# Kernel optimization log

Hardware: AMD Instinct MI355X
Metric: run time of the kernel (lower is better)

The kernel has to match this reference:

```python
import jax, jax.numpy as jnp
import numpy as np

N_NODES = 50000
N_EDGES = 800000
D_IN = 128
D_OUT = 128
ALPHA = 0.5


def setup_inputs() -> dict:
    key = jax.random.key(0)
    k1, k2, k3, k4, k5, k6 = jax.random.split(key, 6)
    x = jax.random.normal(k1, (N_NODES, D_IN), dtype=jnp.float32)
    edge_index = jax.random.randint(k2, (2, N_EDGES), 0, N_NODES, dtype=jnp.int32)
    s = 1.0 / np.sqrt(D_IN)  # torch.nn.Linear default init bound
    W_src = jax.random.uniform(k3, (D_IN, D_OUT), jnp.float32, -s, s)
    b_src = jax.random.uniform(k4, (D_OUT,), jnp.float32, -s, s)
    W_dst = jax.random.uniform(k5, (D_IN, D_OUT), jnp.float32, -s, s)
    b_dst = jax.random.uniform(k6, (D_OUT,), jnp.float32, -s, s)
    return {"x": x, "edge_index": edge_index, "W_src": W_src, "b_src": b_src,
            "W_dst": W_dst, "b_dst": b_dst}


def reference(x, edge_index, W_src, b_src, W_dst, b_dst):
    row, col = edge_index[0], edge_index[1]
    ones = jnp.ones((row.shape[0],), dtype=x.dtype)
    # out-degree = row sums of A; in-degree = column sums of A
    out_deg = jax.ops.segment_sum(ones, row, num_segments=N_NODES)
    in_deg = jax.ops.segment_sum(ones, col, num_segments=N_NODES)
    d_out = jnp.where(out_deg > 0, out_deg ** -0.5, 0.0)
    d_in = jnp.where(in_deg > 0, in_deg ** -0.5, 0.0)
    # D_out^{-1/2} A D_in^{-1/2}: per-edge weight. For A^T the normalized
    # weight at (col,row) is d_in[col]*d_out[row] == same weight, transposed scatter.
    w = d_out[row] * d_in[col]  # [E]
    msg_fwd = w[:, None] * x[col]  # [E, D_IN]
    agg_fwd = jax.ops.segment_sum(msg_fwd, row, num_segments=N_NODES)  # adj_norm @ x
    msg_bwd = w[:, None] * x[row]
    agg_bwd = jax.ops.segment_sum(msg_bwd, col, num_segments=N_NODES)  # adj_t_norm @ x
    out = ALPHA * (agg_fwd @ W_src + b_src) + (1.0 - ALPHA) * (agg_bwd @ W_dst + b_dst)
    return out
```

## Files before the change

### kernel.cpp

```cpp
#include <hip/hip_runtime.h>
#include <hip/hip_bf16.h>


constexpr int N_NODES = 50000;
constexpr int N_EDGES = 800000;
constexpr int D = 128;
constexpr int CAP = 48;
constexpr int NPBK = 512;
constexpr int NBUK = (N_NODES + NPBK - 1) / NPBK;
constexpr int ECH = 2048;
constexpr int NCH = (N_EDGES + ECH - 1) / ECH;
constexpr int CAPB = 12288;

typedef __bf16 bf16x8 __attribute__((ext_vector_type(8)));
typedef float  f32x4  __attribute__((ext_vector_type(4)));

__global__ __launch_bounds__(256) void k_part(const int* __restrict__ row,
                                              const int* __restrict__ col,
                                              int* __restrict__ tail,
                                              unsigned* __restrict__ part,
                                              const float* __restrict__ Wsrc,
                                              const float* __restrict__ Wdst,
                                              __hip_bfloat16* __restrict__ Wpk) {
    const int bid = blockIdx.x;
    if (bid >= NCH * 2) {
        int tid = (bid - NCH * 2) * 256 + threadIdx.x;
        int f = tid >> 6;
        int lane = tid & 63;
        int dir = f >> 5;
        int ct = (f >> 2) & 7;
        int ks = f & 3;
        const float* W = dir ? Wdst : Wsrc;
        int k0 = ks * 32 + (lane >> 4) * 8;
        int n = ct * 16 + (lane & 15);
        __hip_bfloat16 v[8];
        #pragma unroll
        for (int j = 0; j < 8; ++j) v[j] = __float2bfloat16(W[(k0 + j) * D + n]);
        *(bf16x8*)&Wpk[(size_t)tid * 8] = *(const bf16x8*)v;
        return;
    }
    __shared__ int cnt[NBUK], base[NBUK], pos[NBUK];
    const int dir = bid & 1;
    const int chunk = bid >> 1;
    const int* dst = dir ? col : row;
    const int* src = dir ? row : col;
    for (int i = threadIdx.x; i < NBUK; i += 256) { cnt[i] = 0; pos[i] = 0; }
    __syncthreads();
    const int e0 = chunk * ECH;
    const int e1 = min(e0 + ECH, N_EDGES);
    for (int e = e0 + threadIdx.x; e < e1; e += 256)
        atomicAdd(&cnt[dst[e] >> 9], 1);
    __syncthreads();
    for (int i = threadIdx.x; i < NBUK; i += 256)
        base[i] = (cnt[i] > 0) ? atomicAdd(&tail[dir * NBUK + i], cnt[i]) : 0;
    __syncthreads();
    for (int e = e0 + threadIdx.x; e < e1; e += 256) {
        int d = dst[e], s = src[e];
        int b = d >> 9;
        int p = base[b] + atomicAdd(&pos[b], 1);
        if (p < CAPB)
            part[((size_t)dir * NBUK + b) * CAPB + p] =
                ((unsigned)(d & (NPBK - 1)) << 16) | (unsigned)s;
    }
}

__global__ __launch_bounds__(256) void k_bin(const int* __restrict__ tail,
                                             const unsigned* __restrict__ part,
                                             unsigned short* __restrict__ binF,
                                             unsigned short* __restrict__ binB,
                                             int* __restrict__ cntF,
                                             int* __restrict__ cntB,
                                             float* __restrict__ sc_row,
                                             float* __restrict__ sc_col) {
    __shared__ alignas(16) unsigned short bins[NPBK * CAP];
    __shared__ int cnt[NPBK];
    const int dir = blockIdx.x & 1;
    const int b = blockIdx.x >> 1;
    for (int i = threadIdx.x; i < NPBK; i += 256) cnt[i] = 0;
    __syncthreads();
    const int n = min(tail[dir * NBUK + b], CAPB);
    const unsigned* p = &part[((size_t)dir * NBUK + b) * CAPB];
    for (int i = threadIdx.x; i < n; i += 256) {
        unsigned ent = p[i];
        int dl = ent >> 16;
        int q = atomicAdd(&cnt[dl], 1);
        if (q < CAP) bins[dl * CAP + q] = (unsigned short)(ent & 0xFFFFu);
    }
    __syncthreads();
    unsigned short* gbin = dir ? binB : binF;
    int* gcnt = dir ? cntB : cntF;
    float* sc = dir ? sc_col : sc_row;
    const int node0 = b * NPBK;
    const int nv = min(NPBK, N_NODES - node0);
    const int nq = nv * (CAP * 2 / 16);
    const uint4* bw = (const uint4*)bins;
    uint4* gw = (uint4*)&gbin[(size_t)node0 * CAP];
    for (int i = threadIdx.x; i < nq; i += 256) gw[i] = bw[i];
    for (int i = threadIdx.x; i < nv; i += 256) {
        int c = cnt[i];
        gcnt[node0 + i] = c;
        sc[node0 + i] = (c > 0) ? rsqrtf((float)c) : 0.f;
    }
}

__global__ __launch_bounds__(256) void k_gemm_mfma(const float* __restrict__ x,
                                                   const bf16x8* __restrict__ Wpk,
                                                   const float* __restrict__ sc_col,
                                                   const float* __restrict__ sc_row,
                                                   __hip_bfloat16* __restrict__ hF,
                                                   __hip_bfloat16* __restrict__ hB) {
    __shared__ bf16x8 Bs[64 * 64];
    for (int i = threadIdx.x; i < 64 * 64; i += 256) Bs[i] = Wpk[i];

    const int wave = threadIdx.x >> 6;
    const int lane = threadIdx.x & 63;
    const int quad = lane >> 4;
    const int m0 = blockIdx.x * 64 + wave * 16;

    const int arow = min(m0 + (lane & 15), N_NODES - 1);
    bf16x8 a[4];
    #pragma unroll
    for (int ks = 0; ks < 4; ++ks) {
        const float* px = &x[(size_t)arow * D + ks * 32 + quad * 8];
        float4 v0 = *(const float4*)px;
        float4 v1 = *(const float4*)(px + 4);
        union { bf16x8 v; __hip_bfloat16 e[8]; } u;
        u.e[0] = __float2bfloat16(v0.x); u.e[1] = __float2bfloat16(v0.y);
        u.e[2] = __float2bfloat16(v0.z); u.e[3] = __float2bfloat16(v0.w);
        u.e[4] = __float2bfloat16(v1.x); u.e[5] = __float2bfloat16(v1.y);
        u.e[6] = __float2bfloat16(v1.z); u.e[7] = __float2bfloat16(v1.w);
        a[ks] = u.v;
    }

    const int crow = m0 + quad * 4;
    float fF[4], fB[4];
    #pragma unroll
    for (int r = 0; r < 4; ++r) {
        int nd = min(crow + r, N_NODES - 1);
        fF[r] = 0.5f * sc_col[nd];
        fB[r] = 0.5f * sc_row[nd];
    }

    __syncthreads();

    #pragma unroll
    for (int ct = 0; ct < 8; ++ct) {
        f32x4 cF = {0.f, 0.f, 0.f, 0.f};
        f32x4 cB = {0.f, 0.f, 0.f, 0.f};
        #pragma unroll
        for (int ks = 0; ks < 4; ++ks) {
            bf16x8 bF = Bs[(ct * 4 + ks) * 64 + lane];
            bf16x8 bB = Bs[(32 + ct * 4 + ks) * 64 + lane];
            cF = __builtin_amdgcn_mfma_f32_16x16x32_bf16(a[ks], bF, cF, 0, 0, 0);
            cB = __builtin_amdgcn_mfma_f32_16x16x32_bf16(a[ks], bB, cB, 0, 0, 0);
        }
        const int colb = ct * 16 + (lane & 15);
        #pragma unroll
        for (int r = 0; r < 4; ++r) {
            int nd = crow + r;
            if (nd < N_NODES) {
                hF[(size_t)nd * D + colb] = __float2bfloat16(fF[r] * cF[r]);
                hB[(size_t)nd * D + colb] = __float2bfloat16(fB[r] * cB[r]);
            }
        }
    }
}

__device__ __forceinline__ float4 bf4_to_f4(uint2 u) {
    union { unsigned i; float f; } a, b, c, d;
    a.i = u.x << 16;
    b.i = u.x & 0xFFFF0000u;
    c.i = u.y << 16;
    d.i = u.y & 0xFFFF0000u;
    return make_float4(a.f, b.f, c.f, d.f);
}

__global__ __launch_bounds__(256) void k_gather(const unsigned short* __restrict__ binF,
                                                const int* __restrict__ cntF,
                                                const unsigned short* __restrict__ binB,
                                                const int* __restrict__ cntB,
                                                const float* __restrict__ sc_row,
                                                const float* __restrict__ sc_col,
                                                const uint2* __restrict__ hF,
                                                const uint2* __restrict__ hB,
                                                const float* __restrict__ b_src,
                                                const float* __restrict__ b_dst,
                                                float* __restrict__ out) {
    const int node = blockIdx.x * 4 + (threadIdx.x >> 6);
    const int lane = threadIdx.x & 63;
    const int half = lane >> 5;
    const int l32 = lane & 31;
    const int nF = min(cntF[node], CAP);
    const int nB = min(cntB[node], CAP);

    int entF = (lane < nF) ? (int)binF[(size_t)node * CAP + lane] : 0;
    int entB = (lane < nB) ? (int)binB[(size_t)node * CAP + lane] : 0;

    const int sTailF = __shfl(entF, (nF > 0) ? nF - 1 : 0);
    const int sTailB = __shfl(entB, (nB > 0) ? nB - 1 : 0);

    float4 accF = make_float4(0.f, 0.f, 0.f, 0.f);
    {
        const int npair = nF >> 1;
        int i = 0;
        for (; i + 3 < npair; i += 4) {
            int s0 = __shfl(entF, 2 * i + half);
            int s1 = __shfl(entF, 2 * (i + 1) + half);
            int s2 = __shfl(entF, 2 * (i + 2) + half);
            int s3 = __shfl(entF, 2 * (i + 3) + half);
            uint2 v0 = hF[(size_t)s0 * 32 + l32];
            uint2 v1 = hF[(size_t)s1 * 32 + l32];
            uint2 v2 = hF[(size_t)s2 * 32 + l32];
            uint2 v3 = hF[(size_t)s3 * 32 + l32];
            float4 f0 = bf4_to_f4(v0), f1 = bf4_to_f4(v1);
            float4 f2 = bf4_to_f4(v2), f3 = bf4_to_f4(v3);
            accF.x += (f0.x + f1.x) + (f2.x + f3.x);
            accF.y += (f0.y + f1.y) + (f2.y + f3.y);
            accF.z += (f0.z + f1.z) + (f2.z + f3.z);
            accF.w += (f0.w + f1.w) + (f2.w + f3.w);
        }
        for (; i < npair; ++i) {
            int s = __shfl(entF, 2 * i + half);
            float4 f = bf4_to_f4(hF[(size_t)s * 32 + l32]);
            accF.x += f.x; accF.y += f.y; accF.z += f.z; accF.w += f.w;
        }
        if ((nF & 1) && half == 0) {
            float4 f = bf4_to_f4(hF[(size_t)sTailF * 32 + l32]);
            accF.x += f.x; accF.y += f.y; accF.z += f.z; accF.w += f.w;
        }
    }
    float4 accB = make_float4(0.f, 0.f, 0.f, 0.f);
    {
        const int npair = nB >> 1;
        int i = 0;
        for (; i + 3 < npair; i += 4) {
            int s0 = __shfl(entB, 2 * i + half);
            int s1 = __shfl(entB, 2 * (i + 1) + half);
            int s2 = __shfl(entB, 2 * (i + 2) + half);
            int s3 = __shfl(entB, 2 * (i + 3) + half);
            uint2 v0 = hB[(size_t)s0 * 32 + l32];
            uint2 v1 = hB[(size_t)s1 * 32 + l32];
            uint2 v2 = hB[(size_t)s2 * 32 + l32];
            uint2 v3 = hB[(size_t)s3 * 32 + l32];
            float4 f0 = bf4_to_f4(v0), f1 = bf4_to_f4(v1);
            float4 f2 = bf4_to_f4(v2), f3 = bf4_to_f4(v3);
            accB.x += (f0.x + f1.x) + (f2.x + f3.x);
            accB.y += (f0.y + f1.y) + (f2.y + f3.y);
            accB.z += (f0.z + f1.z) + (f2.z + f3.z);
            accB.w += (f0.w + f1.w) + (f2.w + f3.w);
        }
        for (; i < npair; ++i) {
            int s = __shfl(entB, 2 * i + half);
            float4 f = bf4_to_f4(hB[(size_t)s * 32 + l32]);
            accB.x += f.x; accB.y += f.y; accB.z += f.z; accB.w += f.w;
        }
        if ((nB & 1) && half == 0) {
            float4 f = bf4_to_f4(hB[(size_t)sTailB * 32 + l32]);
            accB.x += f.x; accB.y += f.y; accB.z += f.z; accB.w += f.w;
        }
    }

    accF.x += __shfl_xor(accF.x, 32);
    accF.y += __shfl_xor(accF.y, 32);
    accF.z += __shfl_xor(accF.z, 32);
    accF.w += __shfl_xor(accF.w, 32);
    accB.x += __shfl_xor(accB.x, 32);
    accB.y += __shfl_xor(accB.y, 32);
    accB.z += __shfl_xor(accB.z, 32);
    accB.w += __shfl_xor(accB.w, 32);

    if (half == 0) {
        float4 bs = *(const float4*)&b_src[l32 * 4];
        float4 bd = *(const float4*)&b_dst[l32 * 4];
        float sF = sc_row[node];
        float sB = sc_col[node];
        float4 o;
        o.x = 0.5f * (bs.x + bd.x) + sF * accF.x + sB * accB.x;
        o.y = 0.5f * (bs.y + bd.y) + sF * accF.y + sB * accB.y;
        o.z = 0.5f * (bs.z + bd.z) + sF * accF.z + sB * accB.z;
        o.w = 0.5f * (bs.w + bd.w) + sF * accF.w + sB * accB.w;
        *(float4*)&out[(size_t)node * D + l32 * 4] = o;
    }
}

extern "C" void kernel_launch(void* const* d_in, const int* in_sizes, int n_in,
                              void* d_out, int out_size, void* d_ws, size_t ws_size,
                              hipStream_t stream) {
    const float* x     = (const float*)d_in[0];
    const int*   edges = (const int*)d_in[1];
    const float* W_src = (const float*)d_in[2];
    const float* b_src = (const float*)d_in[3];
    const float* W_dst = (const float*)d_in[4];
    const float* b_dst = (const float*)d_in[5];
    float* out = (float*)d_out;

    const int* row = edges;
    const int* col = edges + N_EDGES;

    __hip_bfloat16* hFu    = (__hip_bfloat16*)d_ws;
    __hip_bfloat16* hBu    = hFu + (size_t)N_NODES * D;
    __hip_bfloat16* Wpk    = hBu + (size_t)N_NODES * D;
    float*          sc_row = (float*)(Wpk + 64 * 512);
    float*          sc_col = sc_row + N_NODES;
    int*            cntF   = (int*)(sc_col + N_NODES);
    int*            cntB   = cntF + N_NODES;
    int*            tail   = cntB + N_NODES;
    unsigned*       part   = (unsigned*)(tail + 256);
    unsigned short* binF   = (unsigned short*)(part + (size_t)2 * NBUK * CAPB);
    unsigned short* binB   = binF + (size_t)N_NODES * CAP;

    (void)hipMemsetAsync(tail, 0, 256 * sizeof(int), stream);

    const int gP = NCH * 2 + 16;
    const int gB = NBUK * 2;
    const int gM = (N_NODES + 63) / 64;
    const int gG = N_NODES / 4;

    k_part<<<gP, 256, 0, stream>>>(row, col, tail, part, W_src, W_dst, Wpk);
    k_bin<<<gB, 256, 0, stream>>>(tail, part, binF, binB, cntF, cntB, sc_row, sc_col);
    k_gemm_mfma<<<gM, 256, 0, stream>>>(x, (const bf16x8*)Wpk, sc_col, sc_row, hFu, hBu);
    k_gather<<<gG, 256, 0, stream>>>(binF, cntF, binB, cntB, sc_row, sc_col,
                                     (const uint2*)hFu, (const uint2*)hBu,
                                     b_src, b_dst, out);
}
```

Before: 197.1 us.

## Aggregate before GEMM: gather bf16 x once, then fused dual-weight MFMA GEMM

Reorders the computation to aggregate first and multiply by the weights afterwards. Previously the code projected x through both weight matrices into two bf16 feature tables and then gathered from each. Now x is converted to bf16 once inside the partition kernel, the gather reads that single table for both directions with per-edge source scaling, and a final MFMA kernel multiplies the concatenated aggregates by [W_src; W_dst] and adds the bias. This halves the working set of the random gather. The cost is per-edge weight shuffles, an extra write and read of the aggregates, and reuse of the partition buffer's memory for aggF.

```diff
diff --git a/kernel.cpp b/kernel.cpp
--- a/kernel.cpp
+++ b/kernel.cpp
@@ -11,6 +11,7 @@
 constexpr int ECH = 2048;
 constexpr int NCH = (N_EDGES + ECH - 1) / ECH;
 constexpr int CAPB = 12288;
+constexpr int CVTB = 128;
 
 typedef __bf16 bf16x8 __attribute__((ext_vector_type(8)));
 typedef float  f32x4  __attribute__((ext_vector_type(4)));
@@ -21,8 +22,27 @@
                                               unsigned* __restrict__ part,
                                               const float* __restrict__ Wsrc,
                                               const float* __restrict__ Wdst,
-                                              __hip_bfloat16* __restrict__ Wpk) {
+                                              __hip_bfloat16* __restrict__ Wpk,
+                                              const float* __restrict__ x,
+                                              __hip_bfloat16* __restrict__ xb) {
     const int bid = blockIdx.x;
+    if (bid >= NCH * 2 + 16) {
+        const float4* x4 = (const float4*)x;
+        bf16x8* xb8 = (bf16x8*)xb;
+        const int stride = CVTB * 256;
+        for (int i = (bid - (NCH * 2 + 16)) * 256 + threadIdx.x;
+             i < N_NODES * D / 8; i += stride) {
+            float4 v0 = x4[2 * i];
+            float4 v1 = x4[2 * i + 1];
+            union { bf16x8 v; __hip_bfloat16 e[8]; } u;
+            u.e[0] = __float2bfloat16(v0.x); u.e[1] = __float2bfloat16(v0.y);
+            u.e[2] = __float2bfloat16(v0.z); u.e[3] = __float2bfloat16(v0.w);
+            u.e[4] = __float2bfloat16(v1.x); u.e[5] = __float2bfloat16(v1.y);
+            u.e[6] = __float2bfloat16(v1.z); u.e[7] = __float2bfloat16(v1.w);
+            xb8[i] = u.v;
+        }
+        return;
+    }
     if (bid >= NCH * 2) {
         int tid = (bid - NCH * 2) * 256 + threadIdx.x;
         int f = tid >> 6;
@@ -103,69 +123,6 @@
     }
 }
 
-__global__ __launch_bounds__(256) void k_gemm_mfma(const float* __restrict__ x,
-                                                   const bf16x8* __restrict__ Wpk,
-                                                   const float* __restrict__ sc_col,
-                                                   const float* __restrict__ sc_row,
-                                                   __hip_bfloat16* __restrict__ hF,
-                                                   __hip_bfloat16* __restrict__ hB) {
-    __shared__ bf16x8 Bs[64 * 64];
-    for (int i = threadIdx.x; i < 64 * 64; i += 256) Bs[i] = Wpk[i];
-
-    const int wave = threadIdx.x >> 6;
-    const int lane = threadIdx.x & 63;
-    const int quad = lane >> 4;
-    const int m0 = blockIdx.x * 64 + wave * 16;
-
-    const int arow = min(m0 + (lane & 15), N_NODES - 1);
-    bf16x8 a[4];
-    #pragma unroll
-    for (int ks = 0; ks < 4; ++ks) {
-        const float* px = &x[(size_t)arow * D + ks * 32 + quad * 8];
-        float4 v0 = *(const float4*)px;
-        float4 v1 = *(const float4*)(px + 4);
-        union { bf16x8 v; __hip_bfloat16 e[8]; } u;
-        u.e[0] = __float2bfloat16(v0.x); u.e[1] = __float2bfloat16(v0.y);
-        u.e[2] = __float2bfloat16(v0.z); u.e[3] = __float2bfloat16(v0.w);
-        u.e[4] = __float2bfloat16(v1.x); u.e[5] = __float2bfloat16(v1.y);
-        u.e[6] = __float2bfloat16(v1.z); u.e[7] = __float2bfloat16(v1.w);
-        a[ks] = u.v;
-    }
-
-    const int crow = m0 + quad * 4;
-    float fF[4], fB[4];
-    #pragma unroll
-    for (int r = 0; r < 4; ++r) {
-        int nd = min(crow + r, N_NODES - 1);
-        fF[r] = 0.5f * sc_col[nd];
-        fB[r] = 0.5f * sc_row[nd];
-    }
-
-    __syncthreads();
-
-    #pragma unroll
-    for (int ct = 0; ct < 8; ++ct) {
-        f32x4 cF = {0.f, 0.f, 0.f, 0.f};
-        f32x4 cB = {0.f, 0.f, 0.f, 0.f};
-        #pragma unroll
-        for (int ks = 0; ks < 4; ++ks) {
-            bf16x8 bF = Bs[(ct * 4 + ks) * 64 + lane];
-            bf16x8 bB = Bs[(32 + ct * 4 + ks) * 64 + lane];
-            cF = __builtin_amdgcn_mfma_f32_16x16x32_bf16(a[ks], bF, cF, 0, 0, 0);
-            cB = __builtin_amdgcn_mfma_f32_16x16x32_bf16(a[ks], bB, cB, 0, 0, 0);
-        }
-        const int colb = ct * 16 + (lane & 15);
-        #pragma unroll
-        for (int r = 0; r < 4; ++r) {
-            int nd = crow + r;
-            if (nd < N_NODES) {
-                hF[(size_t)nd * D + colb] = __float2bfloat16(fF[r] * cF[r]);
-                hB[(size_t)nd * D + colb] = __float2bfloat16(fB[r] * cB[r]);
-            }
-        }
-    }
-}
-
 __device__ __forceinline__ float4 bf4_to_f4(uint2 u) {
     union { unsigned i; float f; } a, b, c, d;
     a.i = u.x << 16;
@@ -175,17 +132,24 @@
     return make_float4(a.f, b.f, c.f, d.f);
 }
 
-__global__ __launch_bounds__(256) void k_gather(const unsigned short* __restrict__ binF,
-                                                const int* __restrict__ cntF,
-                                                const unsigned short* __restrict__ binB,
-                                                const int* __restrict__ cntB,
-                                                const float* __restrict__ sc_row,
-                                                const float* __restrict__ sc_col,
-                                                const uint2* __restrict__ hF,
-                                                const uint2* __restrict__ hB,
-                                                const float* __restrict__ b_src,
-                                                const float* __restrict__ b_dst,
-                                                float* __restrict__ out) {
+__device__ __forceinline__ uint2 f4_to_bf4(float4 f) {
+    union { uint2 u; __hip_bfloat16 e[4]; } r;
+    r.e[0] = __float2bfloat16(f.x);
+    r.e[1] = __float2bfloat16(f.y);
+    r.e[2] = __float2bfloat16(f.z);
+    r.e[3] = __float2bfloat16(f.w);
+    return r.u;
+}
+
+__global__ __launch_bounds__(256) void k_agg(const unsigned short* __restrict__ binF,
+                                             const int* __restrict__ cntF,
+                                             const unsigned short* __restrict__ binB,
+                                             const int* __restrict__ cntB,
+                                             const float* __restrict__ sc_row,
+                                             const float* __restrict__ sc_col,
+                                             const uint2* __restrict__ xb,
+                                             __hip_bfloat16* __restrict__ aggF,
+                                             __hip_bfloat16* __restrict__ aggB) {
     const int node = blockIdx.x * 4 + (threadIdx.x >> 6);
     const int lane = threadIdx.x & 63;
     const int half = lane >> 5;
@@ -195,9 +159,13 @@
 
     int entF = (lane < nF) ? (int)binF[(size_t)node * CAP + lane] : 0;
     int entB = (lane < nB) ? (int)binB[(size_t)node * CAP + lane] : 0;
+    float sclF = sc_col[entF];
+    float sclB = sc_row[entB];
 
     const int sTailF = __shfl(entF, (nF > 0) ? nF - 1 : 0);
     const int sTailB = __shfl(entB, (nB > 0) ? nB - 1 : 0);
+    const float wTailF = __shfl(sclF, (nF > 0) ? nF - 1 : 0);
+    const float wTailB = __shfl(sclB, (nB > 0) ? nB - 1 : 0);
 
     float4 accF = make_float4(0.f, 0.f, 0.f, 0.f);
     {
@@ -208,25 +176,32 @@
             int s1 = __shfl(entF, 2 * (i + 1) + half);
             int s2 = __shfl(entF, 2 * (i + 2) + half);
             int s3 = __shfl(entF, 2 * (i + 3) + half);
-            uint2 v0 = hF[(size_t)s0 * 32 + l32];
-            uint2 v1 = hF[(size_t)s1 * 32 + l32];
-            uint2 v2 = hF[(size_t)s2 * 32 + l32];
-            uint2 v3 = hF[(size_t)s3 * 32 + l32];
+            float w0 = __shfl(sclF, 2 * i + half);
+            float w1 = __shfl(sclF, 2 * (i + 1) + half);
+            float w2 = __shfl(sclF, 2 * (i + 2) + half);
+            float w3 = __shfl(sclF, 2 * (i + 3) + half);
+            uint2 v0 = xb[(size_t)s0 * 32 + l32];
+            uint2 v1 = xb[(size_t)s1 * 32 + l32];
+            uint2 v2 = xb[(size_t)s2 * 32 + l32];
+            uint2 v3 = xb[(size_t)s3 * 32 + l32];
             float4 f0 = bf4_to_f4(v0), f1 = bf4_to_f4(v1);
             float4 f2 = bf4_to_f4(v2), f3 = bf4_to_f4(v3);
-            accF.x += (f0.x + f1.x) + (f2.x + f3.x);
-            accF.y += (f0.y + f1.y) + (f2.y + f3.y);
-            accF.z += (f0.z + f1.z) + (f2.z + f3.z);
-            accF.w += (f0.w + f1.w) + (f2.w + f3.w);
+            accF.x += w0 * f0.x + w1 * f1.x + w2 * f2.x + w3 * f3.x;
+            accF.y += w0 * f0.y + w1 * f1.y + w2 * f2.y + w3 * f3.y;
+            accF.z += w0 * f0.z + w1 * f1.z + w2 * f2.z + w3 * f3.z;
+            accF.w += w0 * f0.w + w1 * f1.w + w2 * f2.w + w3 * f3.w;
         }
         for (; i < npair; ++i) {
             int s = __shfl(entF, 2 * i + half);
-            float4 f = bf4_to_f4(hF[(size_t)s * 32 + l32]);
-            accF.x += f.x; accF.y += f.y; accF.z += f.z; accF.w += f.w;
+            float w = __shfl(sclF, 2 * i + half);
+            float4 f = bf4_to_f4(xb[(size_t)s * 32 + l32]);
+            accF.x += w * f.x; accF.y += w * f.y;
+            accF.z += w * f.z; accF.w += w * f.w;
         }
         if ((nF & 1) && half == 0) {
-            float4 f = bf4_to_f4(hF[(size_t)sTailF * 32 + l32]);
-            accF.x += f.x; accF.y += f.y; accF.z += f.z; accF.w += f.w;
+            float4 f = bf4_to_f4(xb[(size_t)sTailF * 32 + l32]);
+            accF.x += wTailF * f.x; accF.y += wTailF * f.y;
+            accF.z += wTailF * f.z; accF.w += wTailF * f.w;
         }
     }
     float4 accB = make_float4(0.f, 0.f, 0.f, 0.f);
@@ -238,25 +213,32 @@
             int s1 = __shfl(entB, 2 * (i + 1) + half);
             int s2 = __shfl(entB, 2 * (i + 2) + half);
             int s3 = __shfl(entB, 2 * (i + 3) + half);
-            uint2 v0 = hB[(size_t)s0 * 32 + l32];
-            uint2 v1 = hB[(size_t)s1 * 32 + l32];
-            uint2 v2 = hB[(size_t)s2 * 32 + l32];
-            uint2 v3 = hB[(size_t)s3 * 32 + l32];
+            float w0 = __shfl(sclB, 2 * i + half);
+            float w1 = __shfl(sclB, 2 * (i + 1) + half);
+            float w2 = __shfl(sclB, 2 * (i + 2) + half);
+            float w3 = __shfl(sclB, 2 * (i + 3) + half);
+            uint2 v0 = xb[(size_t)s0 * 32 + l32];
+            uint2 v1 = xb[(size_t)s1 * 32 + l32];
+            uint2 v2 = xb[(size_t)s2 * 32 + l32];
+            uint2 v3 = xb[(size_t)s3 * 32 + l32];
             float4 f0 = bf4_to_f4(v0), f1 = bf4_to_f4(v1);
             float4 f2 = bf4_to_f4(v2), f3 = bf4_to_f4(v3);
-            accB.x += (f0.x + f1.x) + (f2.x + f3.x);
-            accB.y += (f0.y + f1.y) + (f2.y + f3.y);
-            accB.z += (f0.z + f1.z) + (f2.z + f3.z);
-            accB.w += (f0.w + f1.w) + (f2.w + f3.w);
+            accB.x += w0 * f0.x + w1 * f1.x + w2 * f2.x + w3 * f3.x;
+            accB.y += w0 * f0.y + w1 * f1.y + w2 * f2.y + w3 * f3.y;
+            accB.z += w0 * f0.z + w1 * f1.z + w2 * f2.z + w3 * f3.z;
+            accB.w += w0 * f0.w + w1 * f1.w + w2 * f2.w + w3 * f3.w;
         }
         for (; i < npair; ++i) {
             int s = __shfl(entB, 2 * i + half);
-            float4 f = bf4_to_f4(hB[(size_t)s * 32 + l32]);
-            accB.x += f.x; accB.y += f.y; accB.z += f.z; accB.w += f.w;
+            float w = __shfl(sclB, 2 * i + half);
+            float4 f = bf4_to_f4(xb[(size_t)s * 32 + l32]);
+            accB.x += w * f.x; accB.y += w * f.y;
+            accB.z += w * f.z; accB.w += w * f.w;
         }
         if ((nB & 1) && half == 0) {
-            float4 f = bf4_to_f4(hB[(size_t)sTailB * 32 + l32]);
-            accB.x += f.x; accB.y += f.y; accB.z += f.z; accB.w += f.w;
+            float4 f = bf4_to_f4(xb[(size_t)sTailB * 32 + l32]);
+            accB.x += wTailB * f.x; accB.y += wTailB * f.y;
+            accB.z += wTailB * f.z; accB.w += wTailB * f.w;
         }
     }
 
@@ -270,16 +252,57 @@
     accB.w += __shfl_xor(accB.w, 32);
 
     if (half == 0) {
-        float4 bs = *(const float4*)&b_src[l32 * 4];
-        float4 bd = *(const float4*)&b_dst[l32 * 4];
-        float sF = sc_row[node];
-        float sB = sc_col[node];
-        float4 o;
-        o.x = 0.5f * (bs.x + bd.x) + sF * accF.x + sB * accB.x;
-        o.y = 0.5f * (bs.y + bd.y) + sF * accF.y + sB * accB.y;
-        o.z = 0.5f * (bs.z + bd.z) + sF * accF.z + sB * accB.z;
-        o.w = 0.5f * (bs.w + bd.w) + sF * accF.w + sB * accB.w;
-        *(float4*)&out[(size_t)node * D + l32 * 4] = o;
+        float s = 0.5f * sc_row[node];
+        ((uint2*)aggF)[(size_t)node * 32 + l32] =
+            f4_to_bf4(make_float4(s * accF.x, s * accF.y, s * accF.z, s * accF.w));
+    } else {
+        float s = 0.5f * sc_col[node];
+        ((uint2*)aggB)[(size_t)node * 32 + l32] =
+            f4_to_bf4(make_float4(s * accB.x, s * accB.y, s * accB.z, s * accB.w));
+    }
+}
+
+__global__ __launch_bounds__(256) void k_gemm_out(const __hip_bfloat16* __restrict__ aggF,
+                                                  const __hip_bfloat16* __restrict__ aggB,
+                                                  const bf16x8* __restrict__ Wpk,
+                                                  const float* __restrict__ b_src,
+                                                  const float* __restrict__ b_dst,
+                                                  float* __restrict__ out) {
+    __shared__ bf16x8 Bs[64 * 64];
+    for (int i = threadIdx.x; i < 64 * 64; i += 256) Bs[i] = Wpk[i];
+
+    const int wave = threadIdx.x >> 6;
+    const int lane = threadIdx.x & 63;
+    const int quad = lane >> 4;
+    const int m0 = blockIdx.x * 64 + wave * 16;
+
+    const int arow = min(m0 + (lane & 15), N_NODES - 1);
+    bf16x8 aF[4], aB[4];
+    #pragma unroll
+    for (int ks = 0; ks < 4; ++ks) {
+        aF[ks] = *(const bf16x8*)&aggF[(size_t)arow * D + ks * 32 + quad * 8];
+        aB[ks] = *(const bf16x8*)&aggB[(size_t)arow * D + ks * 32 + quad * 8];
+    }
+
+    __syncthreads();
+
+    const int crow = m0 + quad * 4;
+    #pragma unroll
+    for (int ct = 0; ct < 8; ++ct) {
+        f32x4 c = {0.f, 0.f, 0.f, 0.f};
+        #pragma unroll
+        for (int ks = 0; ks < 4; ++ks)
+            c = __builtin_amdgcn_mfma_f32_16x16x32_bf16(aF[ks], Bs[(ct * 4 + ks) * 64 + lane], c, 0, 0, 0);
+        #pragma unroll
+        for (int ks = 0; ks < 4; ++ks)
+            c = __builtin_amdgcn_mfma_f32_16x16x32_bf16(aB[ks], Bs[(32 + ct * 4 + ks) * 64 + lane], c, 0, 0, 0);
+        const int colb = ct * 16 + (lane & 15);
+        const float bias = 0.5f * (b_src[colb] + b_dst[colb]);
+        #pragma unroll
+        for (int r = 0; r < 4; ++r) {
+            int nd = crow + r;
+            if (nd < N_NODES) out[(size_t)nd * D + colb] = c[r] + bias;
+        }
     }
 }
 
@@ -297,29 +320,30 @@
     const int* row = edges;
     const int* col = edges + N_EDGES;
 
-    __hip_bfloat16* hFu    = (__hip_bfloat16*)d_ws;
-    __hip_bfloat16* hBu    = hFu + (size_t)N_NODES * D;
-    __hip_bfloat16* Wpk    = hBu + (size_t)N_NODES * D;
+    __hip_bfloat16* xb     = (__hip_bfloat16*)d_ws;
+    __hip_bfloat16* aggF   = xb + (size_t)N_NODES * D;
+    __hip_bfloat16* aggB   = aggF + (size_t)N_NODES * D;
+    __hip_bfloat16* Wpk    = aggB + (size_t)N_NODES * D;
     float*          sc_row = (float*)(Wpk + 64 * 512);
     float*          sc_col = sc_row + N_NODES;
     int*            cntF   = (int*)(sc_col + N_NODES);
     int*            cntB   = cntF + N_NODES;
     int*            tail   = cntB + N_NODES;
-    unsigned*       part   = (unsigned*)(tail + 256);
-    unsigned short* binF   = (unsigned short*)(part + (size_t)2 * NBUK * CAPB);
+    unsigned short* binF   = (unsigned short*)(tail + 256);
     unsigned short* binB   = binF + (size_t)N_NODES * CAP;
+    unsigned*       part   = (unsigned*)aggF;
 
     (void)hipMemsetAsync(tail, 0, 256 * sizeof(int), stream);
 
-    const int gP = NCH * 2 + 16;
+    const int gP = NCH * 2 + 16 + CVTB;
     const int gB = NBUK * 2;
+    const int gA = N_NODES / 4;
     const int gM = (N_NODES + 63) / 64;
-    const int gG = N_NODES / 4;
-
-    k_part<<<gP, 256, 0, stream>>>(row, col, tail, part, W_src, W_dst, Wpk);
+
+    k_part<<<gP, 256, 0, stream>>>(row, col, tail, part, W_src, W_dst, Wpk, x, xb);
     k_bin<<<gB, 256, 0, stream>>>(tail, part, binF, binB, cntF, cntB, sc_row, sc_col);
-    k_gemm_mfma<<<gM, 256, 0, stream>>>(x, (const bf16x8*)Wpk, sc_col, sc_row, hFu, hBu);
-    k_gather<<<gG, 256, 0, stream>>>(binF, cntF, binB, cntB, sc_row, sc_col,
-                                     (const uint2*)hFu, (const uint2*)hBu,
-                                     b_src, b_dst, out);
-}
+    k_agg<<<gA, 256, 0, stream>>>(binF, cntF, binB, cntB, sc_row, sc_col,
+                                  (const uint2*)xb, aggF, aggB);
+    k_gemm_out<<<gM, 256, 0, stream>>>(aggF, aggB, (const bf16x8*)Wpk,
+                                       b_src, b_dst, out);
+}
```

After: 198.4 us. Within noise of the previous version (+0.7%).
